# Kernel optimization log

Hardware: AMD Instinct MI355X
Metric: run time of the kernel (lower is better)

## Reference

```python
import jax, jax.numpy as jnp
import numpy as np

NEG_SLOPE = 0.2

def gat_conv(x, src, dst, W, a_src, a_dst, b, num_nodes, concat):
    # PyG GATConv (add_self_loops already applied to src/dst).
    H, C = a_src.shape
    h = (x @ W).reshape(-1, H, C)                      # [N,H,C]
    s = jnp.einsum('nhc,hc->nh', h, a_src)             # per-node src score
    d = jnp.einsum('nhc,hc->nh', h, a_dst)             # per-node dst score
    e = jax.nn.leaky_relu(s[src] + d[dst], NEG_SLOPE)  # [E,H]
    emax = jax.lax.stop_gradient(
        jax.ops.segment_max(e, dst, num_segments=num_nodes))  # [N,H]
    ex = jnp.exp(e - emax[dst])
    denom = jax.ops.segment_sum(ex, dst, num_segments=num_nodes)
    alpha = ex / denom[dst]                            # segment softmax over in-edges
    msg = h[src] * alpha[:, :, None]                   # [E,H,C]
    out = jax.ops.segment_sum(msg, dst, num_segments=num_nodes)
    out = out.reshape(num_nodes, H * C) if concat else out.mean(axis=1)
    return out + b

def setup_inputs() -> dict:
    key = jax.random.key(0)
    ks = jax.random.split(key, 20)
    N, E, F = 50000, 400000, 256
    x = jax.random.normal(ks[0], (N, F), dtype=jnp.float32)
    edge_index = jax.random.randint(ks[1], (2, E), 0, N, dtype=jnp.int64)
    def p(k, shape):
        return (jax.random.normal(k, shape, dtype=jnp.float32) * 0.1)
    inp = {'x': x, 'edge_index': edge_index}
    # conv1: 256 -> 8x32 ; conv2: 256 -> 4x32 ; conv3: 128 -> 2x32 ; conv4: 64 -> 1x32
    dims = [(256, 8, 32), (256, 4, 32), (128, 2, 32), (64, 1, 32)]
    ki = 2
    for i, (fin, H, C) in enumerate(dims, start=1):
        inp[f'W{i}'] = p(ks[ki], (fin, H * C)); ki += 1
        inp[f'a_src{i}'] = p(ks[ki], (H, C)); ki += 1
        inp[f'a_dst{i}'] = p(ks[ki], (H, C)); ki += 1
        bdim = H * C if i < 4 else C
        inp[f'b{i}'] = jnp.zeros((bdim,), dtype=jnp.float32)
    return inp

def reference(x, edge_index, W1, a_src1, a_dst1, b1, W2, a_src2, a_dst2, b2,
              W3, a_src3, a_dst3, b3, W4, a_src4, a_dst4, b4):
    N = x.shape[0]
    loops = jnp.arange(N, dtype=edge_index.dtype)
    src = jnp.concatenate([edge_index[0], loops])
    dst = jnp.concatenate([edge_index[1], loops])
    h = jax.nn.elu(gat_conv(x, src, dst, W1, a_src1, a_dst1, b1, N, True))
    h = jax.nn.elu(gat_conv(h, src, dst, W2, a_src2, a_dst2, b2, N, True))
    h = gat_conv(h, src, dst, W3, a_src3, a_dst3, b3, N, True)
    h = jax.nn.elu(h)
    h = gat_conv(h, src, dst, W4, a_src4, a_dst4, b4, N, False)
    return jax.nn.log_softmax(h, axis=1)
```

## Files before the change

kernel.cpp:

```cpp
#include <hip/hip_runtime.h>
#include <hip/hip_bf16.h>

#define LRELU_SLOPE 0.2f

typedef __attribute__((ext_vector_type(8))) short short8;
typedef __attribute__((ext_vector_type(4))) float f32x4;

__device__ __forceinline__ unsigned short bf16r(float f) {
    unsigned int u = __builtin_bit_cast(unsigned int, f);
    u += 0x7fffu + ((u >> 16) & 1u);
    return (unsigned short)(u >> 16);
}
__device__ __forceinline__ float bf2f(unsigned short u) {
    return __builtin_bit_cast(float, (unsigned int)u << 16);
}


#define WTOT 108544

__global__ void k_pre(const float* __restrict__ Wa, const float* __restrict__ Wb,
                      const float* __restrict__ Wc, const float* __restrict__ Wd,
                      unsigned short* __restrict__ Ta, unsigned short* __restrict__ Tb,
                      unsigned short* __restrict__ Tc, unsigned short* __restrict__ Td,
                      const int* __restrict__ ei, int* __restrict__ cnt, int E, int N) {
    int gid = blockIdx.x * blockDim.x + threadIdx.x;
    if (gid < WTOT) {
        int id = gid;
        const float* W; unsigned short* T; int K, Nc;
        if (id < 65536)       { W = Wa; T = Ta; K = 256; Nc = 256; }
        else if (id < 98304)  { id -= 65536;  W = Wb; T = Tb; K = 256; Nc = 128; }
        else if (id < 106496) { id -= 98304;  W = Wc; T = Tc; K = 128; Nc = 64; }
        else                  { id -= 106496; W = Wd; T = Td; K = 64;  Nc = 32; }
        int n = id / K, k = id % K;
        T[id] = bf16r(W[(long)k * Nc + n]);
        return;
    }
    int e = gid - WTOT;
    if (e >= E + N) return;
    int dst = (e < E) ? ei[E + e] : (e - E);
    atomicAdd(&cnt[dst], 1);
}


__global__ void k_scan_blk(const int* __restrict__ cnt, int* __restrict__ offs,
                           int* __restrict__ bsum, int N) {
    __shared__ int temp[1024];
    int t = threadIdx.x;
    int gi = blockIdx.x * 1024 + t;
    int v = (gi < N) ? cnt[gi] : 0;
    temp[t] = v;
    __syncthreads();
    for (int o = 1; o < 1024; o <<= 1) {
        int x = (t >= o) ? temp[t - o] : 0;
        __syncthreads();
        temp[t] += x;
        __syncthreads();
    }
    if (gi < N) offs[gi] = temp[t] - v;
    if (t == 1023) bsum[blockIdx.x] = temp[1023];
}

__global__ void k_scan(const int* __restrict__ cnt, int* __restrict__ offs, int N) {
    __shared__ int temp[1024];
    __shared__ int carry_s;
    int t = threadIdx.x;
    if (t == 0) carry_s = 0;
    __syncthreads();
    for (int base = 0; base < N; base += 1024) {
        int v = (base + t < N) ? cnt[base + t] : 0;
        temp[t] = v;
        __syncthreads();
        for (int o = 1; o < 1024; o <<= 1) {
            int x = (t >= o) ? temp[t - o] : 0;
            __syncthreads();
            temp[t] += x;
            __syncthreads();
        }
        int incl = temp[t];
        int carry = carry_s;
        if (base + t < N) offs[base + t] = carry + incl - v;
        __syncthreads();
        if (t == 1023) carry_s = carry + temp[1023];
        __syncthreads();
    }
    if (t == 0) offs[N] = carry_s;
}

__global__ void k_scan_add(int* __restrict__ offs, const int* __restrict__ bpre,
                           int* __restrict__ wp, int N, int nb) {
    int gi = blockIdx.x * blockDim.x + threadIdx.x;
    if (gi < N) {
        int v = offs[gi] + bpre[gi >> 10];
        offs[gi] = v;
        wp[gi] = v;
    } else if (gi == N) {
        offs[N] = bpre[nb];
    }
}

__global__ void k_scatter(const int* __restrict__ ei, int* __restrict__ wp,
                          int* __restrict__ adj, int E, int N) {
    int e = blockIdx.x * blockDim.x + threadIdx.x;
    if (e >= E + N) return;
    int srcn = (e < E) ? ei[e] : (e - E);
    int dst  = (e < E) ? ei[E + e] : (e - E);
    int pos = atomicAdd(&wp[dst], 1);
    adj[pos] = srcn;
}


template<int BN, int KT, int GX, bool F32A>
__global__ __launch_bounds__(256) void k_mgemm(const void* __restrict__ Ain,
                                               const unsigned short* __restrict__ WT,
                                               unsigned short* __restrict__ Cb,
                                               const float* __restrict__ a_src,
                                               const float* __restrict__ a_dst,
                                               float* __restrict__ sbuf,
                                               float* __restrict__ dbuf,
                                               int M, int Nc, int H, int RB) {
    constexpr int KITER = KT / 32;
    constexpr int KS  = KT + 8;
    constexpr int NBF = BN / 16;
    constexpr int CPR = BN / 32;
    constexpr int SP  = BN + 8;
    constexpr int STAGE = BN * KS;
    constexpr int EPIL  = 64 * SP;
    constexpr int LBSZ  = STAGE > EPIL ? STAGE : EPIL;
    __shared__ __align__(16) unsigned short LB[LBSZ];

    int id = blockIdx.x;
    int xcd = id & 7;
    int q  = id >> 3;
    int ct = q % GX;
    int rb = (q / GX) * 8 + xcd;
    if (rb >= RB) return;
    int bm = rb * 64, bn = ct * BN;

    int t = threadIdx.x;
    int wv = t >> 6, l = t & 63;
    int row_in = l & 15, quad = l >> 4;

    int grA = min(bm + wv * 16 + row_in, M - 1);
    const float* Af = (const float*)Ain;
    const unsigned short* Ab = (const unsigned short*)Ain;
    float4 af0[KITER], af1[KITER];
    short8 areg[KITER];
    if constexpr (F32A) {
#pragma unroll
        for (int ki = 0; ki < KITER; ++ki) {
            const float4* p = (const float4*)&Af[(long)grA * KT + ki * 32 + quad * 8];
            af0[ki] = p[0];
            af1[ki] = p[1];
        }
    } else {
#pragma unroll
        for (int ki = 0; ki < KITER; ++ki)
            areg[ki] = *(const short8*)&Ab[(long)grA * KT + ki * 32 + quad * 8];
    }

    constexpr int PER = BN * (KT / 8) / 256;
#pragma unroll
    for (int i = 0; i < PER; ++i) {
        int ch = t + i * 256;
        int col = ch / (KT / 8);
        int kc  = ch % (KT / 8);
        int gcol = min(bn + col, Nc - 1);
        *(short8*)&LB[col * KS + kc * 8] = *(const short8*)&WT[(long)gcol * KT + kc * 8];
    }
    __syncthreads();

    f32x4 acc[NBF];
#pragma unroll
    for (int j = 0; j < NBF; ++j) acc[j] = (f32x4){0.f, 0.f, 0.f, 0.f};

#pragma unroll
    for (int ki = 0; ki < KITER; ++ki) {
        short8 av;
        if constexpr (F32A) {
            float4 f0 = af0[ki], f1 = af1[ki];
            av[0] = (short)bf16r(f0.x); av[1] = (short)bf16r(f0.y);
            av[2] = (short)bf16r(f0.z); av[3] = (short)bf16r(f0.w);
            av[4] = (short)bf16r(f1.x); av[5] = (short)bf16r(f1.y);
            av[6] = (short)bf16r(f1.z); av[7] = (short)bf16r(f1.w);
        } else {
            av = areg[ki];
        }
#pragma unroll
        for (int f = 0; f < NBF; ++f) {
            short8 bv = *(const short8*)&LB[(f * 16 + row_in) * KS + ki * 32 + quad * 8];
            acc[f] = __builtin_amdgcn_mfma_f32_16x16x32_bf16(av, bv, acc[f], 0, 0, 0);
        }
    }
    __syncthreads();

#pragma unroll
    for (int r = 0; r < 4; ++r)
#pragma unroll
        for (int f = 0; f < NBF; ++f)
            LB[(wv * 16 + quad * 4 + r) * SP + f * 16 + row_in] = bf16r(acc[f][r]);
    __syncthreads();

    int rr = t / CPR, cc = t % CPR;
    if (rr < 64) {
        int grow = bm + rr;
        int colb = bn + cc * 32;
        if (grow < M && colb < Nc) {
            const unsigned short* ep = &LB[rr * SP + cc * 32];
            short8 v0 = *(const short8*)(ep);
            short8 v1 = *(const short8*)(ep + 8);
            short8 v2 = *(const short8*)(ep + 16);
            short8 v3 = *(const short8*)(ep + 24);
            unsigned short* cp = &Cb[(long)grow * Nc + colb];
            *(short8*)(cp)      = v0;
            *(short8*)(cp + 8)  = v1;
            *(short8*)(cp + 16) = v2;
            *(short8*)(cp + 24) = v3;
            int hd = colb >> 5;
            const float* ap = a_src + hd * 32;
            const float* dp = a_dst + hd * 32;
            float ss = 0.f, dd = 0.f;
#pragma unroll
            for (int u = 0; u < 8; ++u) {
                float va = bf2f((unsigned short)v0[u]); ss += va * ap[u];      dd += va * dp[u];
                float vb = bf2f((unsigned short)v1[u]); ss += vb * ap[8 + u];  dd += vb * dp[8 + u];
                float vc = bf2f((unsigned short)v2[u]); ss += vc * ap[16 + u]; dd += vc * dp[16 + u];
                float vd = bf2f((unsigned short)v3[u]); ss += vd * ap[24 + u]; dd += vd * dp[24 + u];
            }
            sbuf[(long)grow * H + hd] = ss;
            dbuf[(long)grow * H + hd] = dd;
        }
    }
}


template<int ACT>
__global__ void k_aggf(const unsigned short* __restrict__ h, const float* __restrict__ s,
                       const float* __restrict__ dsc, const int* __restrict__ offs,
                       const int* __restrict__ adj, const float* __restrict__ bias,
                       unsigned short* __restrict__ out16, float* __restrict__ out32,
                       int N, int H) {
    const int C8 = 4;
    long tid = (long)blockIdx.x * blockDim.x + threadIdx.x;
    int HC8 = H * C8;
    if (tid >= (long)N * HC8) return;
    int c8 = (int)(tid % C8);
    int hh = (int)((tid / C8) % H);
    int n  = (int)(tid / HC8);
    int beg = offs[n], end = offs[n + 1];
    float dn = dsc[n * H + hh];
    int HC = HC8 * 8;
    int coff = hh * 32 + c8 * 8;

    float denom = 0.f;
    float acc[8];
#pragma unroll
    for (int u = 0; u < 8; ++u) acc[u] = 0.f;

    for (int j = beg; j < end; ++j) {
        int sn = adj[j];
        float e = s[sn * H + hh] + dn;
        e = e > 0.f ? e : LRELU_SLOPE * e;
        float w = __expf(fminf(e, 80.f));
        short8 hv = *(const short8*)(h + (size_t)sn * HC + coff);
        denom += w;
#pragma unroll
        for (int u = 0; u < 8; ++u)
            acc[u] += w * bf2f((unsigned short)hv[u]);
    }

    float inv = 1.0f / denom;
    float o[8];
#pragma unroll
    for (int u = 0; u < 8; ++u) o[u] = acc[u] * inv + bias[coff + u];

    if (ACT == 1) {
        short8 pk;
#pragma unroll
        for (int u = 0; u < 8; ++u) {
            float v = o[u] > 0.f ? o[u] : (__expf(o[u]) - 1.f);
            pk[u] = (short)bf16r(v);
        }
        *(short8*)(out16 + tid * 8) = pk;
    } else {
        float m = o[0];
#pragma unroll
        for (int u = 1; u < 8; ++u) m = fmaxf(m, o[u]);
        m = fmaxf(m, __shfl_xor(m, 1));
        m = fmaxf(m, __shfl_xor(m, 2));
        float ssum = 0.f;
#pragma unroll
        for (int u = 0; u < 8; ++u) ssum += __expf(o[u] - m);
        ssum += __shfl_xor(ssum, 1);
        ssum += __shfl_xor(ssum, 2);
        float lse = m + __logf(ssum);
        float4 lo = {o[0] - lse, o[1] - lse, o[2] - lse, o[3] - lse};
        float4 hi = {o[4] - lse, o[5] - lse, o[6] - lse, o[7] - lse};
        *(float4*)(out32 + tid * 8)     = lo;
        *(float4*)(out32 + tid * 8 + 4) = hi;
    }
}


static inline size_t align_up(size_t x) { return (x + 255) & ~(size_t)255; }

extern "C" void kernel_launch(void* const* d_in, const int* in_sizes, int n_in,
                              void* d_out, int out_size, void* d_ws, size_t ws_size,
                              hipStream_t stream) {
    const float* x   = (const float*)d_in[0];
    const int*   ei  = (const int*)d_in[1];

    const int N = in_sizes[0] / 256;
    const int E = in_sizes[1] / 2;
    const int ET = E + N;
    const int NB = (N + 1023) / 1024;

    size_t off = 0;
    char* ws = (char*)d_ws;
    auto take = [&](size_t bytes) { char* p = ws + off; off += align_up(bytes); return p; };
    int*   offs  = (int*)take((size_t)(N + 1) * 4);
    int*   wp    = (int*)take((size_t)N * 4);
    int*   adj   = (int*)take((size_t)ET * 4);
    int*   bsum  = (int*)take((size_t)(NB + 1) * 4);
    int*   bpre  = (int*)take((size_t)(NB + 1) * 4);
    float* sbuf  = (float*)take((size_t)N * 8 * 4);
    float* dbuf  = (float*)take((size_t)N * 8 * 4);
    unsigned short* Xb = (unsigned short*)take((size_t)N * 256 * 2);
    unsigned short* Yb = (unsigned short*)take((size_t)N * 256 * 2);
    unsigned short* WT0 = (unsigned short*)take((size_t)256 * 256 * 2);
    unsigned short* WT1 = (unsigned short*)take((size_t)256 * 128 * 2);
    unsigned short* WT2 = (unsigned short*)take((size_t)128 * 64 * 2);
    unsigned short* WT3 = (unsigned short*)take((size_t)64 * 32 * 2);
    (void)ws_size;

    hipMemsetAsync(wp, 0, (size_t)N * 4, stream);
    {
        long tot = WTOT + ET;
        k_pre<<<(int)((tot + 255) / 256), 256, 0, stream>>>(
            (const float*)d_in[2], (const float*)d_in[6], (const float*)d_in[10],
            (const float*)d_in[14], WT0, WT1, WT2, WT3, ei, wp, E, N);
        k_scan_blk<<<NB, 1024, 0, stream>>>(wp, offs, bsum, N);
        k_scan<<<1, 1024, 0, stream>>>(bsum, bpre, NB);
        k_scan_add<<<(N + 256) / 256, 256, 0, stream>>>(offs, bpre, wp, N, NB);
        k_scatter<<<(ET + 255) / 256, 256, 0, stream>>>(ei, wp, adj, E, N);
    }

    const float* as_[4] = {(const float*)d_in[3], (const float*)d_in[7],
                           (const float*)d_in[11], (const float*)d_in[15]};
    const float* ad_[4] = {(const float*)d_in[4], (const float*)d_in[8],
                           (const float*)d_in[12], (const float*)d_in[16]};
    const float* b_[4]  = {(const float*)d_in[5], (const float*)d_in[9],
                           (const float*)d_in[13], (const float*)d_in[17]};
    int H_[4] = {8, 4, 2, 1};

    const int RB  = (N + 63) / 64;
    const int RBp = ((RB + 7) / 8) * 8;

    for (int li = 0; li < 4; ++li) {
        int H = H_[li];

        if (li == 0) {
            k_mgemm<64, 256, 4, true><<<4 * RBp, 256, 0, stream>>>(
                x, WT0, Yb, as_[0], ad_[0], sbuf, dbuf, N, 256, H, RB);
        } else if (li == 1) {
            k_mgemm<64, 256, 2, false><<<2 * RBp, 256, 0, stream>>>(
                Xb, WT1, Yb, as_[1], ad_[1], sbuf, dbuf, N, 128, H, RB);
        } else if (li == 2) {
            k_mgemm<64, 128, 1, false><<<RBp, 256, 0, stream>>>(
                Xb, WT2, Yb, as_[2], ad_[2], sbuf, dbuf, N, 64, H, RB);
        } else {
            k_mgemm<32, 64, 1, false><<<RBp, 256, 0, stream>>>(
                Xb, WT3, Yb, as_[3], ad_[3], sbuf, dbuf, N, 32, H, RB);
        }
        {
            long total = (long)N * H * 4;
            int nb = (int)((total + 255) / 256);
            if (li < 3)
                k_aggf<1><<<nb, 256, 0, stream>>>(Yb, sbuf, dbuf, offs, adj, b_[li],
                                                  Xb, nullptr, N, H);
            else
                k_aggf<0><<<nb, 256, 0, stream>>>(Yb, sbuf, dbuf, offs, adj, b_[li],
                                                  nullptr, (float*)d_out, N, H);
        }
    }
}
```

Baseline: 338.9 us.

## Split edge-weight computation across lane quads and unroll aggregation by four

In the aggregation kernel, the four lanes that share a node and head now each compute the score and exp for a different edge. They exchange src indices and weights with ds_swizzle, then each issues four independent gathers per iteration. This removes redundant adj and score loads and exp work per lane and raises memory-level parallelism. The GEMM kernel converts its fp32 A operand to bf16 up front, which frees registers, and adds a min-blocks launch bound. Risks: the swizzle assumes the quad lanes are consecutive in the wave and that every lane reaches the loop together, and the rounding of the summation order changes.

New measurement: 317.8 us. -6.2%, faster.

```diff
diff --git a/kernel.cpp b/kernel.cpp
--- a/kernel.cpp
+++ b/kernel.cpp
@@ -110,7 +110,7 @@
 
 
 template<int BN, int KT, int GX, bool F32A>
-__global__ __launch_bounds__(256) void k_mgemm(const void* __restrict__ Ain,
+__global__ __launch_bounds__(256, 4) void k_mgemm(const void* __restrict__ Ain,
                                                const unsigned short* __restrict__ WT,
                                                unsigned short* __restrict__ Cb,
                                                const float* __restrict__ a_src,
@@ -143,14 +143,24 @@
     int grA = min(bm + wv * 16 + row_in, M - 1);
     const float* Af = (const float*)Ain;
     const unsigned short* Ab = (const unsigned short*)Ain;
-    float4 af0[KITER], af1[KITER];
     short8 areg[KITER];
     if constexpr (F32A) {
+        float4 af0[KITER], af1[KITER];
 #pragma unroll
         for (int ki = 0; ki < KITER; ++ki) {
             const float4* p = (const float4*)&Af[(long)grA * KT + ki * 32 + quad * 8];
             af0[ki] = p[0];
             af1[ki] = p[1];
+        }
+#pragma unroll
+        for (int ki = 0; ki < KITER; ++ki) {
+            float4 f0 = af0[ki], f1 = af1[ki];
+            short8 av;
+            av[0] = (short)bf16r(f0.x); av[1] = (short)bf16r(f0.y);
+            av[2] = (short)bf16r(f0.z); av[3] = (short)bf16r(f0.w);
+            av[4] = (short)bf16r(f1.x); av[5] = (short)bf16r(f1.y);
+            av[6] = (short)bf16r(f1.z); av[7] = (short)bf16r(f1.w);
+            areg[ki] = av;
         }
     } else {
 #pragma unroll
@@ -175,16 +185,7 @@
 
 #pragma unroll
     for (int ki = 0; ki < KITER; ++ki) {
-        short8 av;
-        if constexpr (F32A) {
-            float4 f0 = af0[ki], f1 = af1[ki];
-            av[0] = (short)bf16r(f0.x); av[1] = (short)bf16r(f0.y);
-            av[2] = (short)bf16r(f0.z); av[3] = (short)bf16r(f0.w);
-            av[4] = (short)bf16r(f1.x); av[5] = (short)bf16r(f1.y);
-            av[6] = (short)bf16r(f1.z); av[7] = (short)bf16r(f1.w);
-        } else {
-            av = areg[ki];
-        }
+        short8 av = areg[ki];
 #pragma unroll
         for (int f = 0; f < NBF; ++f) {
             short8 bv = *(const short8*)&LB[(f * 16 + row_in) * KS + ki * 32 + quad * 8];
@@ -233,6 +234,8 @@
 }
 
 
+#define QB(v, k) __builtin_amdgcn_ds_swizzle((v), 0x8000 | ((k) * 0x55))
+
 template<int ACT>
 __global__ void k_aggf(const unsigned short* __restrict__ h, const float* __restrict__ s,
                        const float* __restrict__ dsc, const int* __restrict__ offs,
@@ -250,22 +253,41 @@
     float dn = dsc[n * H + hh];
     int HC = HC8 * 8;
     int coff = hh * 32 + c8 * 8;
+    const unsigned short* hb = h + coff;
 
     float denom = 0.f;
     float acc[8];
 #pragma unroll
     for (int u = 0; u < 8; ++u) acc[u] = 0.f;
 
-    for (int j = beg; j < end; ++j) {
-        int sn = adj[j];
+    for (int j = beg; j < end; j += 4) {
+        int my = j + c8;
+        int idx = my < end ? my : end - 1;
+        int sn = adj[idx];
         float e = s[sn * H + hh] + dn;
         e = e > 0.f ? e : LRELU_SLOPE * e;
         float w = __expf(fminf(e, 80.f));
-        short8 hv = *(const short8*)(h + (size_t)sn * HC + coff);
-        denom += w;
-#pragma unroll
-        for (int u = 0; u < 8; ++u)
-            acc[u] += w * bf2f((unsigned short)hv[u]);
+        if (my >= end) w = 0.f;
+        int wi = __builtin_bit_cast(int, w);
+        int sn0 = QB(sn, 0);
+        int sn1 = QB(sn, 1);
+        int sn2 = QB(sn, 2);
+        int sn3 = QB(sn, 3);
+        float w0 = __builtin_bit_cast(float, QB(wi, 0));
+        float w1 = __builtin_bit_cast(float, QB(wi, 1));
+        float w2 = __builtin_bit_cast(float, QB(wi, 2));
+        float w3 = __builtin_bit_cast(float, QB(wi, 3));
+        short8 h0 = *(const short8*)(hb + (size_t)sn0 * HC);
+        short8 h1 = *(const short8*)(hb + (size_t)sn1 * HC);
+        short8 h2 = *(const short8*)(hb + (size_t)sn2 * HC);
+        short8 h3 = *(const short8*)(hb + (size_t)sn3 * HC);
+        denom += (w0 + w1) + (w2 + w3);
+#pragma unroll
+        for (int u = 0; u < 8; ++u) {
+            float a01 = w0 * bf2f((unsigned short)h0[u]) + w1 * bf2f((unsigned short)h1[u]);
+            float a23 = w2 * bf2f((unsigned short)h2[u]) + w3 * bf2f((unsigned short)h3[u]);
+            acc[u] += a01 + a23;
+        }
     }
 
     float inv = 1.0f / denom;
```
